# Kernel tuning notes

Measured on AMD Instinct MI355X. Metric: run time of the kernel, lower is better.

The kernel has to match this reference:

```python
import jax, jax.numpy as jnp
import numpy as np

EPS = 1e-12  # F.normalize eps


def _gather_nb(var, idx):
    # var: [B, N, C], idx: [B, N, K] -> [B, N, K, C]; out[b,n,k,c] = var[b, idx[b,n,k], c]
    return jnp.take_along_axis(var[:, :, None, :], idx[:, :, :, None], axis=1)


def _l2norm(v):
    n = jnp.sqrt(jnp.sum(v * v, axis=-1, keepdims=True))
    return v / jnp.maximum(n, EPS)


def setup_inputs() -> dict:
    key = jax.random.key(0)
    ks = jax.random.split(key, 16)
    B, N, K, dim, hid = 4, 4096, 16, 128, 64
    s = 0.05
    return {
        "pos": jax.random.normal(ks[0], (B, N, 3), jnp.float32),
        "x": jax.random.normal(ks[1], (B, dim, N), jnp.float32),
        "idx": jax.random.randint(ks[2], (B, N, K), 0, N, jnp.int64),
        "dist": jax.random.uniform(ks[3], (B, N, K), jnp.float32),
        "W_qkv": jax.random.normal(ks[4], (3 * dim, dim), jnp.float32) * s,
        "W1": jax.random.normal(ks[5], (hid, 10), jnp.float32) * s,
        "b1": jax.random.normal(ks[6], (hid,), jnp.float32) * s,
        "W2": jax.random.normal(ks[7], (dim, hid), jnp.float32) * s,
        "b2": jax.random.normal(ks[8], (dim,), jnp.float32) * s,
        "Wm1": jax.random.normal(ks[9], (4 * dim, dim), jnp.float32) * s,
        "bm1": jax.random.normal(ks[10], (4 * dim,), jnp.float32) * s,
        "Wm2": jax.random.normal(ks[11], (dim, 4 * dim), jnp.float32) * s,
        "bm2": jax.random.normal(ks[12], (dim,), jnp.float32) * s,
    }


def reference(pos, x, idx, dist, W_qkv, W1, b1, W2, b2, Wm1, bm1, Wm2, bm2):
    B, _, N = x.shape
    xt = jnp.transpose(x, (0, 2, 1))                      # [B, N, C]
    qkv = xt @ W_qkv.T                                    # [B, N, 3C]
    Q, K_, V = jnp.split(qkv, 3, axis=-1)

    Qg = _gather_nb(Q, idx)                               # [B, N, K, C]
    Kg = _gather_nb(K_, idx)
    Vg = _gather_nb(V, idx)

    # position embedding: [center(3) | neighbor(3) | diff(3) | dist(1)] -> MLP 10->hid->C
    pos_nb = _gather_nb(pos, idx)                         # [B, N, K, 3]
    pos_c = jnp.broadcast_to(pos[:, :, None, :], pos_nb.shape)
    feat10 = jnp.concatenate(
        [pos_c, pos_nb, pos_c - pos_nb, dist[..., None]], axis=-1)  # [B, N, K, 10]
    pos_emb = jax.nn.relu(feat10 @ W1.T + b1) @ W2.T + b2  # [B, N, K, C]

    Knorm = _l2norm(Kg + pos_emb)                         # [B, N, K, C]
    Vrel = jax.nn.relu(Vg + pos_emb)                      # [B, N, K, C]
    Qn = _l2norm(Qg)                                      # [B, N, K, C]

    # kv_context: contract over N per neighbor slot k -> [B, K, C, C]
    kv = jnp.einsum('bnkc,bnkd->bkcd', Knorm, Vrel)
    # (1/N) Qn @ kv, then sum over k -> [B, N, C]
    agg = jnp.einsum('bnkc,bkcd->bnd', Qn, kv) / N

    out = jax.nn.relu(agg @ Wm1.T + bm1) @ Wm2.T + bm2 + xt  # [B, N, C]
    return jnp.transpose(out, (0, 2, 1))                     # [B, C, N]
```

## Files before the change

kernel.cpp:

```cpp
#include <hip/hip_runtime.h>
#include <math.h>

#define Bn 4
#define Nn 4096
#define Kn 16
#define Cn 128
#define HIDn 64

#define OFF_WQKVBF 0
#define OFF_WM1BF  24576
#define OFF_WM2BF  57344
#define OFF_W2BFG  90112
#define OFF_QNBF   94208
#define OFF_KMBF   1142784
#define OFF_VMBF   2191360
#define OFF_KVT32  3239936
#define OFF_KVTBF  4288512
#define OFF_AGG0   4812800
#define OFF_AGG1   6909952
#define OFF_FLAG   9007104

typedef short bf16x8 __attribute__((ext_vector_type(8)));
typedef float f32x4 __attribute__((ext_vector_type(4)));

__device__ inline unsigned short f2bf(float f) {
  union { float f; unsigned u; } v; v.f = f;
  unsigned r = v.u + 0x7fffu + ((v.u >> 16) & 1u);
  return (unsigned short)(r >> 16);
}
__device__ inline float b2f(unsigned short s) {
  union { unsigned u; float f; } v; v.u = ((unsigned)s) << 16; return v.f;
}

__global__ void k0_prep(const float* __restrict__ Wqkv,
                        const float* __restrict__ Wm1, const float* __restrict__ Wm2,
                        const float* __restrict__ W2,
                        const int* __restrict__ idx_raw, float* ws) {
  if (blockIdx.x == 0 && threadIdx.x == 0) {
    int any = 0;
    for (int i = 0; i < 64; ++i) any |= idx_raw[2 * i + 1];
    ((int*)(ws + OFF_FLAG))[0] = (any == 0) ? 1 : 0;
  }
  int t = blockIdx.x * 256 + threadIdx.x;
  if (t < 49152) { ((unsigned short*)(ws + OFF_WQKVBF))[t] = f2bf(Wqkv[t]); return; }
  t -= 49152;
  if (t < 65536) { ((unsigned short*)(ws + OFF_WM1BF))[t] = f2bf(Wm1[t]); return; }
  t -= 65536;
  if (t < 65536) { ((unsigned short*)(ws + OFF_WM2BF))[t] = f2bf(Wm2[t]); return; }
  t -= 65536;
  if (t < 8192) { ((unsigned short*)(ws + OFF_W2BFG))[t] = f2bf(W2[t]); return; }
}

__global__ __launch_bounds__(256, 2) void k1_qkv(const float* __restrict__ x, float* ws) {
  __shared__ __align__(16) unsigned short a_lds[32 * 136];
  __shared__ __align__(16) float qkv_lds[32 * 388];
  const unsigned short* Wq = (const unsigned short*)(ws + OFF_WQKVBF);
  unsigned short* Qnbf = (unsigned short*)(ws + OFF_QNBF);
  unsigned short* KmBF = (unsigned short*)(ws + OFF_KMBF);
  unsigned short* VmBF = (unsigned short*)(ws + OFF_VMBF);
  int b = blockIdx.x >> 7;
  int n0 = (blockIdx.x & 127) << 5;
  int t = threadIdx.x;
  int w = t >> 6, l = t & 63, ml = l & 15, gq = l >> 4;
#pragma unroll
  for (int i = 0; i < 16; ++i) {
    int id = t + 256 * i;
    int c = id >> 5, j = id & 31;
    a_lds[j * 136 + c] = f2bf(x[(b * Cn + c) * Nn + n0 + j]);
  }
  __syncthreads();
  f32x4 acc[2][6];
#pragma unroll
  for (int i = 0; i < 2; ++i)
#pragma unroll
    for (int j = 0; j < 6; ++j) acc[i][j] = (f32x4)0.f;
#pragma unroll
  for (int kc = 0; kc < 4; ++kc) {
    bf16x8 av0 = *(const bf16x8*)&a_lds[ml * 136 + kc * 32 + 8 * gq];
    bf16x8 av1 = *(const bf16x8*)&a_lds[(ml + 16) * 136 + kc * 32 + 8 * gq];
#pragma unroll
    for (int nf = 0; nf < 6; ++nf) {
      int m = 96 * w + 16 * nf + ml;
      bf16x8 bv = *(const bf16x8*)&Wq[m * 128 + kc * 32 + 8 * gq];
      acc[0][nf] = __builtin_amdgcn_mfma_f32_16x16x32_bf16(av0, bv, acc[0][nf], 0, 0, 0);
      acc[1][nf] = __builtin_amdgcn_mfma_f32_16x16x32_bf16(av1, bv, acc[1][nf], 0, 0, 0);
    }
  }
#pragma unroll
  for (int mf = 0; mf < 2; ++mf)
#pragma unroll
    for (int nf = 0; nf < 6; ++nf)
#pragma unroll
      for (int r = 0; r < 4; ++r)
        qkv_lds[(16 * mf + 4 * gq + r) * 388 + 96 * w + 16 * nf + ml] = acc[mf][nf][r];
  __syncthreads();
  {
    int g = t >> 3, l8 = t & 7;
    float4 q4[4];
    float ss = 0.f;
#pragma unroll
    for (int q = 0; q < 4; ++q) {
      q4[q] = *(const float4*)&qkv_lds[g * 388 + l8 * 16 + 4 * q];
      ss = fmaf(q4[q].x, q4[q].x, ss); ss = fmaf(q4[q].y, q4[q].y, ss);
      ss = fmaf(q4[q].z, q4[q].z, ss); ss = fmaf(q4[q].w, q4[q].w, ss);
    }
    ss += __shfl_xor(ss, 1); ss += __shfl_xor(ss, 2); ss += __shfl_xor(ss, 4);
    float sc = 1.f / fmaxf(sqrtf(ss), 1e-12f);
    union { unsigned short us[8]; uint4 u4; } o0, o1;
#pragma unroll
    for (int q = 0; q < 2; ++q) {
      o0.us[q * 4 + 0] = f2bf(q4[q].x * sc); o0.us[q * 4 + 1] = f2bf(q4[q].y * sc);
      o0.us[q * 4 + 2] = f2bf(q4[q].z * sc); o0.us[q * 4 + 3] = f2bf(q4[q].w * sc);
    }
#pragma unroll
    for (int q = 0; q < 2; ++q) {
      o1.us[q * 4 + 0] = f2bf(q4[2 + q].x * sc); o1.us[q * 4 + 1] = f2bf(q4[2 + q].y * sc);
      o1.us[q * 4 + 2] = f2bf(q4[2 + q].z * sc); o1.us[q * 4 + 3] = f2bf(q4[2 + q].w * sc);
    }
    *(uint4*)&Qnbf[(b * Nn + n0 + g) * Cn + l8 * 16] = o0.u4;
    *(uint4*)&Qnbf[(b * Nn + n0 + g) * Cn + l8 * 16 + 8] = o1.u4;
  }
#pragma unroll
  for (int i = 0; i < 2; ++i) {
    int id = t + 256 * i;
    int row = id >> 4, c8 = id & 15;
    const float* kp = &qkv_lds[row * 388 + 128 + c8 * 8];
    const float* vp = &qkv_lds[row * 388 + 256 + c8 * 8];
    union { unsigned short us[8]; uint4 u4; } ko, vo;
#pragma unroll
    for (int j = 0; j < 8; ++j) { ko.us[j] = f2bf(kp[j]); vo.us[j] = f2bf(vp[j]); }
    *(uint4*)&KmBF[(b * Nn + n0 + row) * Cn + c8 * 8] = ko.u4;
    *(uint4*)&VmBF[(b * Nn + n0 + row) * Cn + c8 * 8] = vo.u4;
  }
}

#define CH2 8
__global__ __launch_bounds__(256, 2) void k2_kv(const float* __restrict__ pos,
                                                const float* __restrict__ dist,
                                                const int* __restrict__ idxp,
                                                const float* __restrict__ W1,
                                                const float* __restrict__ b1,
                                                const float* __restrict__ b2,
                                                float* ws) {
  __shared__ __align__(16) unsigned short h_lds[32 * 72];
  __shared__ __align__(16) unsigned short pe_bf[32 * 136];
  __shared__ __align__(16) unsigned short K_rm[32 * 136];
  __shared__ __align__(16) unsigned short V_rm[32 * 136];
  __shared__ __align__(16) unsigned short KnT[128 * 40];
  __shared__ __align__(16) unsigned short VrT[128 * 40];

  const unsigned short* KmBF = (const unsigned short*)(ws + OFF_KMBF);
  const unsigned short* VmBF = (const unsigned short*)(ws + OFF_VMBF);
  const unsigned short* W2g = (const unsigned short*)(ws + OFF_W2BFG);
  float* kvt = ws + OFF_KVT32;
  int flag = ((const int*)(ws + OFF_FLAG))[0];

  int bid = blockIdx.x;
  int b = bid & 3;
  int rest = bid >> 2;
  int k = rest & 15, ch = rest >> 4;
  int t = threadIdx.x;
  int w = t >> 6, l = t & 63;
  int ml = l & 15, gq = l >> 4;

  int g = t >> 3, l8 = t & 7;
  int nl = (t >> 3) & 7, half = t & 7;
  int n_b2 = 8 * w + nl;
  int side = t >> 7, cc = t & 127;

  f32x4 acc[2][8];
#pragma unroll
  for (int i = 0; i < 2; ++i)
#pragma unroll
    for (int j = 0; j < 8; ++j) acc[i][j] = (f32x4)0.f;

  int nbase = ch * 512;
  int fidx_m = (b * Nn + nbase + g) * Kn + k;
  int jn_m = flag ? idxp[2 * fidx_m] : idxp[fidx_m];
  float dd = dist[fidx_m];
  float pc0 = pos[(b * Nn + nbase + g) * 3 + 0];
  float pc1 = pos[(b * Nn + nbase + g) * 3 + 1];
  float pc2 = pos[(b * Nn + nbase + g) * 3 + 2];
  float pn0 = pos[(b * Nn + jn_m) * 3 + 0];
  float pn1 = pos[(b * Nn + jn_m) * 3 + 1];
  float pn2 = pos[(b * Nn + jn_m) * 3 + 2];
  int fidx_b = (b * Nn + nbase + n_b2) * Kn + k;
  int jn_b = flag ? idxp[2 * fidx_b] : idxp[fidx_b];
  union U8 { unsigned short us[8]; uint4 u4; };
  U8 ka, kb, va, vb;
  {
    const unsigned short* krow = &KmBF[(b * Nn + jn_b) * Cn];
    const unsigned short* vrow = &VmBF[(b * Nn + jn_b) * Cn];
    ka.u4 = *(const uint4*)&krow[half * 16];
    kb.u4 = *(const uint4*)&krow[half * 16 + 8];
    va.u4 = *(const uint4*)&vrow[half * 16];
    vb.u4 = *(const uint4*)&vrow[half * 16 + 8];
  }

  for (int it = 0; it < 16; ++it) {
    {
      float f10[10] = {pc0, pc1, pc2, pn0, pn1, pn2, pc0 - pn0, pc1 - pn1, pc2 - pn2, dd};
      union { unsigned short us[8]; uint4 u4; } hv;
#pragma unroll
      for (int oo = 0; oo < 8; ++oo) {
        int o = l8 * 8 + oo;
        float a = b1[o];
#pragma unroll
        for (int i2 = 0; i2 < 10; ++i2) a = fmaf(W1[o * 10 + i2], f10[i2], a);
        hv.us[oo] = f2bf(fmaxf(a, 0.f));
      }
      *(uint4*)&h_lds[g * 72 + l8 * 8] = hv.u4;
    }
    int itn = (it < 15) ? it + 1 : 15;
    int n0n = nbase + itn * 32;
    int fidx_mn = (b * Nn + n0n + g) * Kn + k;
    int jn_mn = flag ? idxp[2 * fidx_mn] : idxp[fidx_mn];
    float ddn = dist[fidx_mn];
    int fidx_bn = (b * Nn + n0n + n_b2) * Kn + k;
    int jn_bn = flag ? idxp[2 * fidx_bn] : idxp[fidx_bn];
    __syncthreads();
    {
      f32x4 pacc[2][2];
#pragma unroll
      for (int i = 0; i < 2; ++i)
#pragma unroll
        for (int j = 0; j < 2; ++j) pacc[i][j] = (f32x4)0.f;
#pragma unroll
      for (int hc = 0; hc < 64; hc += 32) {
        bf16x8 av[2];
#pragma unroll
        for (int mf = 0; mf < 2; ++mf)
          av[mf] = *(const bf16x8*)&h_lds[(ml + 16 * mf) * 72 + hc + 8 * gq];
#pragma unroll
        for (int nf = 0; nf < 2; ++nf) {
          int c = 32 * w + 16 * nf + ml;
          bf16x8 bv = *(const bf16x8*)&W2g[c * 64 + hc + 8 * gq];
          pacc[0][nf] = __builtin_amdgcn_mfma_f32_16x16x32_bf16(av[0], bv, pacc[0][nf], 0, 0, 0);
          pacc[1][nf] = __builtin_amdgcn_mfma_f32_16x16x32_bf16(av[1], bv, pacc[1][nf], 0, 0, 0);
        }
      }
#pragma unroll
      for (int mf = 0; mf < 2; ++mf)
#pragma unroll
        for (int nf = 0; nf < 2; ++nf) {
          int c = 32 * w + 16 * nf + ml;
#pragma unroll
          for (int r = 0; r < 4; ++r)
            pe_bf[(16 * mf + 4 * gq + r) * 136 + c] = f2bf(pacc[mf][nf][r]);
        }
    }
    __syncthreads();
    {
      U8 pa, pb;
      pa.u4 = *(const uint4*)&pe_bf[n_b2 * 136 + half * 16];
      pb.u4 = *(const uint4*)&pe_bf[n_b2 * 136 + half * 16 + 8];
      const float4* b2v4 = (const float4*)b2;
      float4 bz[4];
#pragma unroll
      for (int q = 0; q < 4; ++q) bz[q] = b2v4[half * 4 + q];
      float kr[16], vr[16];
      float ss = 0.f;
#pragma unroll
      for (int j = 0; j < 16; ++j) {
        float b2j = (j & 2) ? ((j & 1) ? bz[j >> 2].w : bz[j >> 2].z)
                            : ((j & 1) ? bz[j >> 2].y : bz[j >> 2].x);
        float pe = b2f((j < 8) ? pa.us[j] : pb.us[j - 8]) + b2j;
        float kg = b2f((j < 8) ? ka.us[j] : kb.us[j - 8]);
        float vg = b2f((j < 8) ? va.us[j] : vb.us[j - 8]);
        kr[j] = kg + pe;
        vr[j] = fmaxf(vg + pe, 0.f);
        ss = fmaf(kr[j], kr[j], ss);
      }
      ss += __shfl_xor(ss, 1); ss += __shfl_xor(ss, 2); ss += __shfl_xor(ss, 4);
      float sc = 1.f / fmaxf(sqrtf(ss), 1e-12f);
      union { unsigned short us[8]; uint4 u4; } o;
#pragma unroll
      for (int hh = 0; hh < 2; ++hh) {
#pragma unroll
        for (int j = 0; j < 8; ++j) o.us[j] = f2bf(kr[hh * 8 + j] * sc);
        *(uint4*)&K_rm[n_b2 * 136 + half * 16 + 8 * hh] = o.u4;
      }
#pragma unroll
      for (int hh = 0; hh < 2; ++hh) {
#pragma unroll
        for (int j = 0; j < 8; ++j) o.us[j] = f2bf(vr[hh * 8 + j]);
        *(uint4*)&V_rm[n_b2 * 136 + half * 16 + 8 * hh] = o.u4;
      }
    }
    float pc0n = pos[(b * Nn + n0n + g) * 3 + 0];
    float pc1n = pos[(b * Nn + n0n + g) * 3 + 1];
    float pc2n = pos[(b * Nn + n0n + g) * 3 + 2];
    float pn0n = pos[(b * Nn + jn_mn) * 3 + 0];
    float pn1n = pos[(b * Nn + jn_mn) * 3 + 1];
    float pn2n = pos[(b * Nn + jn_mn) * 3 + 2];
    U8 kan, kbn, van, vbn;
    {
      const unsigned short* krow = &KmBF[(b * Nn + jn_bn) * Cn];
      const unsigned short* vrow = &VmBF[(b * Nn + jn_bn) * Cn];
      kan.u4 = *(const uint4*)&krow[half * 16];
      kbn.u4 = *(const uint4*)&krow[half * 16 + 8];
      van.u4 = *(const uint4*)&vrow[half * 16];
      vbn.u4 = *(const uint4*)&vrow[half * 16 + 8];
    }
    __syncthreads();
    {
      const unsigned short* src = side ? V_rm : K_rm;
      unsigned short* dst = side ? VrT : KnT;
      unsigned v[16];
#pragma unroll
      for (int i = 0; i < 16; ++i) {
        unsigned lo = src[(2 * i) * 136 + cc];
        unsigned hi = src[(2 * i + 1) * 136 + cc];
        v[i] = lo | (hi << 16);
      }
#pragma unroll
      for (int i = 0; i < 4; ++i) {
        uint4 pk = {v[4 * i], v[4 * i + 1], v[4 * i + 2], v[4 * i + 3]};
        *(uint4*)&dst[cc * 40 + 8 * i] = pk;
      }
    }
    __syncthreads();
    {
      bf16x8 av[2];
#pragma unroll
      for (int mf = 0; mf < 2; ++mf)
        av[mf] = *(const bf16x8*)&VrT[(32 * w + 16 * mf + ml) * 40 + 8 * gq];
#pragma unroll
      for (int nf = 0; nf < 8; ++nf) {
        bf16x8 bv = *(const bf16x8*)&KnT[(16 * nf + ml) * 40 + 8 * gq];
#pragma unroll
        for (int mf = 0; mf < 2; ++mf)
          acc[mf][nf] = __builtin_amdgcn_mfma_f32_16x16x32_bf16(av[mf], bv, acc[mf][nf], 0, 0, 0);
      }
    }
    dd = ddn;
    pc0 = pc0n; pc1 = pc1n; pc2 = pc2n;
    pn0 = pn0n; pn1 = pn1n; pn2 = pn2n;
    ka.u4 = kan.u4; kb.u4 = kbn.u4; va.u4 = van.u4; vb.u4 = vbn.u4;
  }
  float* kvp = kvt + (b * Kn + k) * Cn * Cn;
#pragma unroll
  for (int mf = 0; mf < 2; ++mf)
#pragma unroll
    for (int nf = 0; nf < 8; ++nf) {
      int c = 16 * nf + ml;
#pragma unroll
      for (int r = 0; r < 4; ++r) {
        int d = 32 * w + 16 * mf + 4 * gq + r;
        atomicAdd(&kvp[d * Cn + c], acc[mf][nf][r]);
      }
    }
}

__global__ __launch_bounds__(256) void k2b_cvt(float* ws) {
  const float* src = ws + OFF_KVT32;
  unsigned short* dst = (unsigned short*)(ws + OFF_KVTBF);
  int i = blockIdx.x * 256 + threadIdx.x;
  float4 a = *(const float4*)&src[i * 8];
  float4 c = *(const float4*)&src[i * 8 + 4];
  union { unsigned short us[8]; uint4 u4; } o;
  o.us[0] = f2bf(a.x); o.us[1] = f2bf(a.y); o.us[2] = f2bf(a.z); o.us[3] = f2bf(a.w);
  o.us[4] = f2bf(c.x); o.us[5] = f2bf(c.y); o.us[6] = f2bf(c.z); o.us[7] = f2bf(c.w);
  *(uint4*)&dst[i * 8] = o.u4;
}

__global__ __launch_bounds__(256, 4) void k3_agg(const int* __restrict__ idxp, float* ws) {
  __shared__ __align__(16) unsigned short qt[32 * 136];
  const unsigned short* Qnbf = (const unsigned short*)(ws + OFF_QNBF);
  const unsigned short* kvtbf = (const unsigned short*)(ws + OFF_KVTBF);
  int flag = ((const int*)(ws + OFF_FLAG))[0];

  int bid = blockIdx.x;
  int b = bid & 3;
  int kh = (bid >> 2) & 1;
  int nt = bid >> 3;
  int n0 = nt * 32;
  int t = threadIdx.x;
  int w = t >> 6, l = t & 63;
  int ml = l & 15, gq = l >> 4;

  f32x4 acc[2][2];
#pragma unroll
  for (int i = 0; i < 2; ++i)
#pragma unroll
    for (int j = 0; j < 2; ++j) acc[i][j] = (f32x4)0.f;

  for (int kk = 0; kk < 8; ++kk) {
    int k = kh * 8 + kk;
    __syncthreads();
#pragma unroll
    for (int i = 0; i < 2; ++i) {
      int id = t + 256 * i;
      int row = id >> 4, c16 = id & 15;
      int fidx = (b * Nn + n0 + row) * Kn + k;
      int jn = flag ? idxp[2 * fidx] : idxp[fidx];
      uint4 v = *(const uint4*)&Qnbf[(b * Nn + jn) * Cn + c16 * 8];
      *(uint4*)&qt[row * 136 + c16 * 8] = v;
    }
    __syncthreads();
    const unsigned short* kvp = &kvtbf[(b * Kn + k) * Cn * Cn];
#pragma unroll
    for (int c0 = 0; c0 < 128; c0 += 32) {
      bf16x8 a0 = *(const bf16x8*)&qt[ml * 136 + c0 + 8 * gq];
      bf16x8 a1 = *(const bf16x8*)&qt[(ml + 16) * 136 + c0 + 8 * gq];
#pragma unroll
      for (int nf = 0; nf < 2; ++nf) {
        int d = 32 * w + 16 * nf + ml;
        bf16x8 bv = *(const bf16x8*)&kvp[d * Cn + c0 + 8 * gq];
        acc[0][nf] = __builtin_amdgcn_mfma_f32_16x16x32_bf16(a0, bv, acc[0][nf], 0, 0, 0);
        acc[1][nf] = __builtin_amdgcn_mfma_f32_16x16x32_bf16(a1, bv, acc[1][nf], 0, 0, 0);
      }
    }
  }
  float* ag = ws + (kh ? OFF_AGG1 : OFF_AGG0);
#pragma unroll
  for (int mf = 0; mf < 2; ++mf)
#pragma unroll
    for (int nf = 0; nf < 2; ++nf) {
      int d = 32 * w + 16 * nf + ml;
#pragma unroll
      for (int r = 0; r < 4; ++r) {
        int n = n0 + 16 * mf + 4 * gq + r;
        ag[(b * Nn + n) * Cn + d] = acc[mf][nf][r];
      }
    }
}

__global__ __launch_bounds__(256, 2) void k4_mlp(const float* __restrict__ x,
                                                 const float* __restrict__ bm1,
                                                 const float* __restrict__ bm2,
                                                 float* __restrict__ out, float* ws) {
  __shared__ __align__(16) unsigned short a_lds[32 * 136];
  __shared__ __align__(16) unsigned short h_lds[32 * 520];
  __shared__ float out_s[128 * 33];
  const float* agg0 = ws + OFF_AGG0;
  const float* agg1 = ws + OFF_AGG1;
  const unsigned short* Wm1bf = (const unsigned short*)(ws + OFF_WM1BF);
  const unsigned short* Wm2bf = (const unsigned short*)(ws + OFF_WM2BF);
  const float invN = 1.f / (float)Nn;
  int b = blockIdx.x >> 7;
  int n0 = (blockIdx.x & 127) << 5;
  int t = threadIdx.x;
  int w = t >> 6, l = t & 63, ml = l & 15, gq = l >> 4;
#pragma unroll
  for (int i = 0; i < 4; ++i) {
    int id = t + 256 * i;
    int row = id >> 5, c4 = id & 31;
    int off = (b * Nn + n0 + row) * Cn + c4 * 4;
    float4 v0 = *(const float4*)&agg0[off];
    float4 v1 = *(const float4*)&agg1[off];
    union { unsigned short us[4]; uint2 u2; } o;
    o.us[0] = f2bf((v0.x + v1.x) * invN); o.us[1] = f2bf((v0.y + v1.y) * invN);
    o.us[2] = f2bf((v0.z + v1.z) * invN); o.us[3] = f2bf((v0.w + v1.w) * invN);
    *(uint2*)&a_lds[row * 136 + c4 * 4] = o.u2;
  }
  __syncthreads();
  {
    f32x4 hacc[2][8];
#pragma unroll
    for (int i = 0; i < 2; ++i)
#pragma unroll
      for (int j = 0; j < 8; ++j) hacc[i][j] = (f32x4)0.f;
#pragma unroll
    for (int kc = 0; kc < 4; ++kc) {
      bf16x8 av0 = *(const bf16x8*)&a_lds[ml * 136 + kc * 32 + 8 * gq];
      bf16x8 av1 = *(const bf16x8*)&a_lds[(ml + 16) * 136 + kc * 32 + 8 * gq];
#pragma unroll
      for (int nf = 0; nf < 8; ++nf) {
        int h = 128 * w + 16 * nf + ml;
        bf16x8 bv = *(const bf16x8*)&Wm1bf[h * 128 + kc * 32 + 8 * gq];
        hacc[0][nf] = __builtin_amdgcn_mfma_f32_16x16x32_bf16(av0, bv, hacc[0][nf], 0, 0, 0);
        hacc[1][nf] = __builtin_amdgcn_mfma_f32_16x16x32_bf16(av1, bv, hacc[1][nf], 0, 0, 0);
      }
    }
#pragma unroll
    for (int mf = 0; mf < 2; ++mf)
#pragma unroll
      for (int nf = 0; nf < 8; ++nf) {
        int h = 128 * w + 16 * nf + ml;
        float bias = bm1[h];
#pragma unroll
        for (int r = 0; r < 4; ++r)
          h_lds[(16 * mf + 4 * gq + r) * 520 + h] = f2bf(fmaxf(hacc[mf][nf][r] + bias, 0.f));
      }
  }
  __syncthreads();
  {
    f32x4 oacc[2][2];
#pragma unroll
    for (int i = 0; i < 2; ++i)
#pragma unroll
      for (int j = 0; j < 2; ++j) oacc[i][j] = (f32x4)0.f;
#pragma unroll
    for (int kc = 0; kc < 16; ++kc) {
      bf16x8 av0 = *(const bf16x8*)&h_lds[ml * 520 + kc * 32 + 8 * gq];
      bf16x8 av1 = *(const bf16x8*)&h_lds[(ml + 16) * 520 + kc * 32 + 8 * gq];
#pragma unroll
      for (int nf = 0; nf < 2; ++nf) {
        int co = 32 * w + 16 * nf + ml;
        bf16x8 bv = *(const bf16x8*)&Wm2bf[co * 512 + kc * 32 + 8 * gq];
        oacc[0][nf] = __builtin_amdgcn_mfma_f32_16x16x32_bf16(av0, bv, oacc[0][nf], 0, 0, 0);
        oacc[1][nf] = __builtin_amdgcn_mfma_f32_16x16x32_bf16(av1, bv, oacc[1][nf], 0, 0, 0);
      }
    }
#pragma unroll
    for (int mf = 0; mf < 2; ++mf)
#pragma unroll
      for (int nf = 0; nf < 2; ++nf) {
        int co = 32 * w + 16 * nf + ml;
        float bias = bm2[co];
#pragma unroll
        for (int r = 0; r < 4; ++r)
          out_s[co * 33 + 16 * mf + 4 * gq + r] = oacc[mf][nf][r] + bias;
      }
  }
  __syncthreads();
#pragma unroll
  for (int i = 0; i < 16; ++i) {
    int id = t + 256 * i;
    int co = id >> 5, j = id & 31;
    out[(b * Cn + co) * Nn + n0 + j] = out_s[co * 33 + j] + x[(b * Cn + co) * Nn + n0 + j];
  }
}

extern "C" void kernel_launch(void* const* d_in, const int* in_sizes, int n_in,
                              void* d_out, int out_size, void* d_ws, size_t ws_size,
                              hipStream_t stream) {
  const float* pos  = (const float*)d_in[0];
  const float* x    = (const float*)d_in[1];
  const int*   idx  = (const int*)d_in[2];
  const float* dist = (const float*)d_in[3];
  const float* Wqkv = (const float*)d_in[4];
  const float* W1   = (const float*)d_in[5];
  const float* b1   = (const float*)d_in[6];
  const float* W2   = (const float*)d_in[7];
  const float* b2   = (const float*)d_in[8];
  const float* Wm1  = (const float*)d_in[9];
  const float* bm1  = (const float*)d_in[10];
  const float* Wm2  = (const float*)d_in[11];
  const float* bm2  = (const float*)d_in[12];
  float* out = (float*)d_out;
  float* ws = (float*)d_ws;

  hipMemsetAsync(ws + OFF_KVT32, 0, (size_t)Bn * Kn * Cn * Cn * sizeof(float), stream);
  hipLaunchKernelGGL(k0_prep, dim3(736), dim3(256), 0, stream, Wqkv, Wm1, Wm2, W2, idx, ws);
  hipLaunchKernelGGL(k1_qkv, dim3(Bn * 128), dim3(256), 0, stream, x, ws);
  hipLaunchKernelGGL(k2_kv, dim3(Bn * Kn * CH2), dim3(256), 0, stream, pos, dist, idx, W1, b1, b2, ws);
  hipLaunchKernelGGL(k2b_cvt, dim3(512), dim3(256), 0, stream, ws);
  hipLaunchKernelGGL(k3_agg, dim3(Bn * 2 * 128), dim3(256), 0, stream, idx, ws);
  hipLaunchKernelGGL(k4_mlp, dim3(Bn * 128), dim3(256), 0, stream, x, bm1, bm2, out, ws);
}
```

Baseline: 167.2 us.

## Compute position-MLP first layer with MFMA and fold biases into epilogues

The scalar FMA loop for the 10->64 position-embedding layer, which read W1 from global memory on every iteration, is replaced by bf16 MFMA over a zero-padded 32-wide feature tile kept in LDS. A new padded bf16 copy of W1 is built in the prep kernel. Biases b1 and b2 are loaded once into registers and added in the MFMA epilogues, and the position gathers are now done by only 32 threads per block. Launch bounds are raised to 3 blocks per CU. The first layer now runs in bf16 (features and weights rounded), which loses some precision, and an extra barrier is added per iteration.

```diff
diff --git a/kernel.cpp b/kernel.cpp
--- a/kernel.cpp
+++ b/kernel.cpp
@@ -11,14 +11,15 @@
 #define OFF_WM1BF  24576
 #define OFF_WM2BF  57344
 #define OFF_W2BFG  90112
-#define OFF_QNBF   94208
-#define OFF_KMBF   1142784
-#define OFF_VMBF   2191360
-#define OFF_KVT32  3239936
-#define OFF_KVTBF  4288512
-#define OFF_AGG0   4812800
-#define OFF_AGG1   6909952
-#define OFF_FLAG   9007104
+#define OFF_W1PBF  94208
+#define OFF_QNBF   95232
+#define OFF_KMBF   1143808
+#define OFF_VMBF   2192384
+#define OFF_KVT32  3240960
+#define OFF_KVTBF  4289536
+#define OFF_AGG0   4813824
+#define OFF_AGG1   6910976
+#define OFF_FLAG   9008128
 
 typedef short bf16x8 __attribute__((ext_vector_type(8)));
 typedef float f32x4 __attribute__((ext_vector_type(4)));
@@ -34,7 +35,7 @@
 
 __global__ void k0_prep(const float* __restrict__ Wqkv,
                         const float* __restrict__ Wm1, const float* __restrict__ Wm2,
-                        const float* __restrict__ W2,
+                        const float* __restrict__ W2, const float* __restrict__ W1,
                         const int* __restrict__ idx_raw, float* ws) {
   if (blockIdx.x == 0 && threadIdx.x == 0) {
     int any = 0;
@@ -49,6 +50,12 @@
   if (t < 65536) { ((unsigned short*)(ws + OFF_WM2BF))[t] = f2bf(Wm2[t]); return; }
   t -= 65536;
   if (t < 8192) { ((unsigned short*)(ws + OFF_W2BFG))[t] = f2bf(W2[t]); return; }
+  t -= 8192;
+  if (t < 2048) {
+    int o = t >> 5, i = t & 31;
+    ((unsigned short*)(ws + OFF_W1PBF))[t] = (i < 10) ? f2bf(W1[o * 10 + i]) : 0;
+    return;
+  }
 }
 
 __global__ __launch_bounds__(256, 2) void k1_qkv(const float* __restrict__ x, float* ws) {
@@ -135,13 +142,13 @@
 }
 
 #define CH2 8
-__global__ __launch_bounds__(256, 2) void k2_kv(const float* __restrict__ pos,
+__global__ __launch_bounds__(256, 3) void k2_kv(const float* __restrict__ pos,
                                                 const float* __restrict__ dist,
                                                 const int* __restrict__ idxp,
-                                                const float* __restrict__ W1,
                                                 const float* __restrict__ b1,
                                                 const float* __restrict__ b2,
                                                 float* ws) {
+  __shared__ __align__(16) unsigned short feat[32 * 40];
   __shared__ __align__(16) unsigned short h_lds[32 * 72];
   __shared__ __align__(16) unsigned short pe_bf[32 * 136];
   __shared__ __align__(16) unsigned short K_rm[32 * 136];
@@ -152,6 +159,7 @@
   const unsigned short* KmBF = (const unsigned short*)(ws + OFF_KMBF);
   const unsigned short* VmBF = (const unsigned short*)(ws + OFF_VMBF);
   const unsigned short* W2g = (const unsigned short*)(ws + OFF_W2BFG);
+  const unsigned short* W1P = (const unsigned short*)(ws + OFF_W1PBF);
   float* kvt = ws + OFF_KVT32;
   int flag = ((const int*)(ws + OFF_FLAG))[0];
 
@@ -163,10 +171,14 @@
   int w = t >> 6, l = t & 63;
   int ml = l & 15, gq = l >> 4;
 
-  int g = t >> 3, l8 = t & 7;
   int nl = (t >> 3) & 7, half = t & 7;
   int n_b2 = 8 * w + nl;
   int side = t >> 7, cc = t & 127;
+  bool is32 = (t < 32);
+
+  float b1v = b1[16 * w + ml];
+  float b2v0 = b2[32 * w + ml];
+  float b2v1 = b2[32 * w + 16 + ml];
 
   f32x4 acc[2][8];
 #pragma unroll
@@ -175,18 +187,22 @@
     for (int j = 0; j < 8; ++j) acc[i][j] = (f32x4)0.f;
 
   int nbase = ch * 512;
-  int fidx_m = (b * Nn + nbase + g) * Kn + k;
-  int jn_m = flag ? idxp[2 * fidx_m] : idxp[fidx_m];
-  float dd = dist[fidx_m];
-  float pc0 = pos[(b * Nn + nbase + g) * 3 + 0];
-  float pc1 = pos[(b * Nn + nbase + g) * 3 + 1];
-  float pc2 = pos[(b * Nn + nbase + g) * 3 + 2];
-  float pn0 = pos[(b * Nn + jn_m) * 3 + 0];
-  float pn1 = pos[(b * Nn + jn_m) * 3 + 1];
-  float pn2 = pos[(b * Nn + jn_m) * 3 + 2];
+  union U8 { unsigned short us[8]; uint4 u4; };
+
+  float dd = 0.f, pc0 = 0.f, pc1 = 0.f, pc2 = 0.f, pn0 = 0.f, pn1 = 0.f, pn2 = 0.f;
+  if (is32) {
+    int fidx_m = (b * Nn + nbase + t) * Kn + k;
+    int jn_m = flag ? idxp[2 * fidx_m] : idxp[fidx_m];
+    dd = dist[fidx_m];
+    pc0 = pos[(b * Nn + nbase + t) * 3 + 0];
+    pc1 = pos[(b * Nn + nbase + t) * 3 + 1];
+    pc2 = pos[(b * Nn + nbase + t) * 3 + 2];
+    pn0 = pos[(b * Nn + jn_m) * 3 + 0];
+    pn1 = pos[(b * Nn + jn_m) * 3 + 1];
+    pn2 = pos[(b * Nn + jn_m) * 3 + 2];
+  }
   int fidx_b = (b * Nn + nbase + n_b2) * Kn + k;
   int jn_b = flag ? idxp[2 * fidx_b] : idxp[fidx_b];
-  union U8 { unsigned short us[8]; uint4 u4; };
   U8 ka, kb, va, vb;
   {
     const unsigned short* krow = &KmBF[(b * Nn + jn_b) * Cn];
@@ -196,26 +212,46 @@
     va.u4 = *(const uint4*)&vrow[half * 16];
     vb.u4 = *(const uint4*)&vrow[half * 16 + 8];
   }
+  if (is32) {
+    float f10[10] = {pc0, pc1, pc2, pn0, pn1, pn2, pc0 - pn0, pc1 - pn1, pc2 - pn2, dd};
+    U8 f0, f1, z;
+#pragma unroll
+    for (int j = 0; j < 8; ++j) f0.us[j] = f2bf(f10[j]);
+    f1.us[0] = f2bf(f10[8]); f1.us[1] = f2bf(f10[9]);
+#pragma unroll
+    for (int j = 2; j < 8; ++j) f1.us[j] = 0;
+#pragma unroll
+    for (int j = 0; j < 8; ++j) z.us[j] = 0;
+    *(uint4*)&feat[t * 40] = f0.u4;
+    *(uint4*)&feat[t * 40 + 8] = f1.u4;
+    *(uint4*)&feat[t * 40 + 16] = z.u4;
+    *(uint4*)&feat[t * 40 + 24] = z.u4;
+  }
 
   for (int it = 0; it < 16; ++it) {
+    __syncthreads();
     {
-      float f10[10] = {pc0, pc1, pc2, pn0, pn1, pn2, pc0 - pn0, pc1 - pn1, pc2 - pn2, dd};
-      union { unsigned short us[8]; uint4 u4; } hv;
-#pragma unroll
-      for (int oo = 0; oo < 8; ++oo) {
-        int o = l8 * 8 + oo;
-        float a = b1[o];
-#pragma unroll
-        for (int i2 = 0; i2 < 10; ++i2) a = fmaf(W1[o * 10 + i2], f10[i2], a);
-        hv.us[oo] = f2bf(fmaxf(a, 0.f));
-      }
-      *(uint4*)&h_lds[g * 72 + l8 * 8] = hv.u4;
+      bf16x8 fa0 = *(const bf16x8*)&feat[ml * 40 + 8 * gq];
+      bf16x8 fa1 = *(const bf16x8*)&feat[(ml + 16) * 40 + 8 * gq];
+      bf16x8 wv = *(const bf16x8*)&W1P[(16 * w + ml) * 32 + 8 * gq];
+      f32x4 h0 = (f32x4)0.f, h1 = (f32x4)0.f;
+      h0 = __builtin_amdgcn_mfma_f32_16x16x32_bf16(fa0, wv, h0, 0, 0, 0);
+      h1 = __builtin_amdgcn_mfma_f32_16x16x32_bf16(fa1, wv, h1, 0, 0, 0);
+#pragma unroll
+      for (int r = 0; r < 4; ++r) {
+        h_lds[(4 * gq + r) * 72 + 16 * w + ml] = f2bf(fmaxf(h0[r] + b1v, 0.f));
+        h_lds[(16 + 4 * gq + r) * 72 + 16 * w + ml] = f2bf(fmaxf(h1[r] + b1v, 0.f));
+      }
     }
     int itn = (it < 15) ? it + 1 : 15;
     int n0n = nbase + itn * 32;
-    int fidx_mn = (b * Nn + n0n + g) * Kn + k;
-    int jn_mn = flag ? idxp[2 * fidx_mn] : idxp[fidx_mn];
-    float ddn = dist[fidx_mn];
+    int jn_mn = 0;
+    float ddn = 0.f;
+    if (is32) {
+      int fidx_mn = (b * Nn + n0n + t) * Kn + k;
+      jn_mn = flag ? idxp[2 * fidx_mn] : idxp[fidx_mn];
+      ddn = dist[fidx_mn];
+    }
     int fidx_bn = (b * Nn + n0n + n_b2) * Kn + k;
     int jn_bn = flag ? idxp[2 * fidx_bn] : idxp[fidx_bn];
     __syncthreads();
@@ -244,9 +280,10 @@
 #pragma unroll
         for (int nf = 0; nf < 2; ++nf) {
           int c = 32 * w + 16 * nf + ml;
+          float bias = nf ? b2v1 : b2v0;
 #pragma unroll
           for (int r = 0; r < 4; ++r)
-            pe_bf[(16 * mf + 4 * gq + r) * 136 + c] = f2bf(pacc[mf][nf][r]);
+            pe_bf[(16 * mf + 4 * gq + r) * 136 + c] = f2bf(pacc[mf][nf][r] + bias);
         }
     }
     __syncthreads();
@@ -254,17 +291,11 @@
       U8 pa, pb;
       pa.u4 = *(const uint4*)&pe_bf[n_b2 * 136 + half * 16];
       pb.u4 = *(const uint4*)&pe_bf[n_b2 * 136 + half * 16 + 8];
-      const float4* b2v4 = (const float4*)b2;
-      float4 bz[4];
-#pragma unroll
-      for (int q = 0; q < 4; ++q) bz[q] = b2v4[half * 4 + q];
       float kr[16], vr[16];
       float ss = 0.f;
 #pragma unroll
       for (int j = 0; j < 16; ++j) {
-        float b2j = (j & 2) ? ((j & 1) ? bz[j >> 2].w : bz[j >> 2].z)
-                            : ((j & 1) ? bz[j >> 2].y : bz[j >> 2].x);
-        float pe = b2f((j < 8) ? pa.us[j] : pb.us[j - 8]) + b2j;
+        float pe = b2f((j < 8) ? pa.us[j] : pb.us[j - 8]);
         float kg = b2f((j < 8) ? ka.us[j] : kb.us[j - 8]);
         float vg = b2f((j < 8) ? va.us[j] : vb.us[j - 8]);
         kr[j] = kg + pe;
@@ -287,12 +318,15 @@
         *(uint4*)&V_rm[n_b2 * 136 + half * 16 + 8 * hh] = o.u4;
       }
     }
-    float pc0n = pos[(b * Nn + n0n + g) * 3 + 0];
-    float pc1n = pos[(b * Nn + n0n + g) * 3 + 1];
-    float pc2n = pos[(b * Nn + n0n + g) * 3 + 2];
-    float pn0n = pos[(b * Nn + jn_mn) * 3 + 0];
-    float pn1n = pos[(b * Nn + jn_mn) * 3 + 1];
-    float pn2n = pos[(b * Nn + jn_mn) * 3 + 2];
+    float pc0n = 0.f, pc1n = 0.f, pc2n = 0.f, pn0n = 0.f, pn1n = 0.f, pn2n = 0.f;
+    if (is32) {
+      pc0n = pos[(b * Nn + n0n + t) * 3 + 0];
+      pc1n = pos[(b * Nn + n0n + t) * 3 + 1];
+      pc2n = pos[(b * Nn + n0n + t) * 3 + 2];
+      pn0n = pos[(b * Nn + jn_mn) * 3 + 0];
+      pn1n = pos[(b * Nn + jn_mn) * 3 + 1];
+      pn2n = pos[(b * Nn + jn_mn) * 3 + 2];
+    }
     U8 kan, kbn, van, vbn;
     {
       const unsigned short* krow = &KmBF[(b * Nn + jn_bn) * Cn];
@@ -333,9 +367,22 @@
           acc[mf][nf] = __builtin_amdgcn_mfma_f32_16x16x32_bf16(av[mf], bv, acc[mf][nf], 0, 0, 0);
       }
     }
-    dd = ddn;
-    pc0 = pc0n; pc1 = pc1n; pc2 = pc2n;
-    pn0 = pn0n; pn1 = pn1n; pn2 = pn2n;
+    if (is32) {
+      float f10[10] = {pc0n, pc1n, pc2n, pn0n, pn1n, pn2n,
+                       pc0n - pn0n, pc1n - pn1n, pc2n - pn2n, ddn};
+      U8 f0, f1, z;
+#pragma unroll
+      for (int j = 0; j < 8; ++j) f0.us[j] = f2bf(f10[j]);
+      f1.us[0] = f2bf(f10[8]); f1.us[1] = f2bf(f10[9]);
+#pragma unroll
+      for (int j = 2; j < 8; ++j) f1.us[j] = 0;
+#pragma unroll
+      for (int j = 0; j < 8; ++j) z.us[j] = 0;
+      *(uint4*)&feat[t * 40] = f0.u4;
+      *(uint4*)&feat[t * 40 + 8] = f1.u4;
+      *(uint4*)&feat[t * 40 + 16] = z.u4;
+      *(uint4*)&feat[t * 40 + 24] = z.u4;
+    }
     ka.u4 = kan.u4; kb.u4 = kbn.u4; va.u4 = van.u4; vb.u4 = vbn.u4;
   }
   float* kvp = kvt + (b * Kn + k) * Cn * Cn;
@@ -543,9 +590,9 @@
   float* ws = (float*)d_ws;
 
   hipMemsetAsync(ws + OFF_KVT32, 0, (size_t)Bn * Kn * Cn * Cn * sizeof(float), stream);
-  hipLaunchKernelGGL(k0_prep, dim3(736), dim3(256), 0, stream, Wqkv, Wm1, Wm2, W2, idx, ws);
+  hipLaunchKernelGGL(k0_prep, dim3(744), dim3(256), 0, stream, Wqkv, Wm1, Wm2, W2, W1, idx, ws);
   hipLaunchKernelGGL(k1_qkv, dim3(Bn * 128), dim3(256), 0, stream, x, ws);
-  hipLaunchKernelGGL(k2_kv, dim3(Bn * Kn * CH2), dim3(256), 0, stream, pos, dist, idx, W1, b1, b2, ws);
+  hipLaunchKernelGGL(k2_kv, dim3(Bn * Kn * CH2), dim3(256), 0, stream, pos, dist, idx, b1, b2, ws);
   hipLaunchKernelGGL(k2b_cvt, dim3(512), dim3(256), 0, stream, ws);
   hipLaunchKernelGGL(k3_agg, dim3(Bn * 2 * 128), dim3(256), 0, stream, idx, ws);
   hipLaunchKernelGGL(k4_mlp, dim3(Bn * 128), dim3(256), 0, stream, x, bm1, bm2, out, ws);
```

Result: slower. 172.3 us (+3.0%).

## Double-buffer transposed K/V tiles and defer kv MFMA to next iteration

Applied to the files above, without the earlier changes.

Double-buffers the transposed KnT/VrT shared tiles in k2_kv. The kv MFMA for tile it-1 now runs at the start of iteration it, which removes one __syncthreads per iteration and lets that MFMA overlap the position-embedding work; a final MFMA after the loop handles the last tile. It also folds the b2 bias into the bf16 conversion of the position embedding instead of reloading b2 per element. Shared memory grows by about 20KB per block, which may limit occupancy at two blocks per CU. Adding the bias before bf16 rounding changes rounding slightly. The workspace offsets shift by 1024 floats.

```diff
diff --git a/kernel.cpp b/kernel.cpp
--- a/kernel.cpp
+++ b/kernel.cpp
@@ -11,14 +11,14 @@
 #define OFF_WM1BF  24576
 #define OFF_WM2BF  57344
 #define OFF_W2BFG  90112
-#define OFF_QNBF   94208
-#define OFF_KMBF   1142784
-#define OFF_VMBF   2191360
-#define OFF_KVT32  3239936
-#define OFF_KVTBF  4288512
-#define OFF_AGG0   4812800
-#define OFF_AGG1   6909952
-#define OFF_FLAG   9007104
+#define OFF_QNBF   95232
+#define OFF_KMBF   1143808
+#define OFF_VMBF   2192384
+#define OFF_KVT32  3240960
+#define OFF_KVTBF  4289536
+#define OFF_AGG0   4813824
+#define OFF_AGG1   6910976
+#define OFF_FLAG   9008128
 
 typedef short bf16x8 __attribute__((ext_vector_type(8)));
 typedef float f32x4 __attribute__((ext_vector_type(4)));
@@ -146,8 +146,8 @@
   __shared__ __align__(16) unsigned short pe_bf[32 * 136];
   __shared__ __align__(16) unsigned short K_rm[32 * 136];
   __shared__ __align__(16) unsigned short V_rm[32 * 136];
-  __shared__ __align__(16) unsigned short KnT[128 * 40];
-  __shared__ __align__(16) unsigned short VrT[128 * 40];
+  __shared__ __align__(16) unsigned short KnT[2][128 * 40];
+  __shared__ __align__(16) unsigned short VrT[2][128 * 40];
 
   const unsigned short* KmBF = (const unsigned short*)(ws + OFF_KMBF);
   const unsigned short* VmBF = (const unsigned short*)(ws + OFF_VMBF);
@@ -168,6 +168,9 @@
   int n_b2 = 8 * w + nl;
   int side = t >> 7, cc = t & 127;
 
+  float b2v0 = b2[32 * w + ml];
+  float b2v1 = b2[32 * w + 16 + ml];
+
   f32x4 acc[2][8];
 #pragma unroll
   for (int i = 0; i < 2; ++i)
@@ -175,6 +178,8 @@
     for (int j = 0; j < 8; ++j) acc[i][j] = (f32x4)0.f;
 
   int nbase = ch * 512;
+  union U8 { unsigned short us[8]; uint4 u4; };
+
   int fidx_m = (b * Nn + nbase + g) * Kn + k;
   int jn_m = flag ? idxp[2 * fidx_m] : idxp[fidx_m];
   float dd = dist[fidx_m];
@@ -186,7 +191,6 @@
   float pn2 = pos[(b * Nn + jn_m) * 3 + 2];
   int fidx_b = (b * Nn + nbase + n_b2) * Kn + k;
   int jn_b = flag ? idxp[2 * fidx_b] : idxp[fidx_b];
-  union U8 { unsigned short us[8]; uint4 u4; };
   U8 ka, kb, va, vb;
   {
     const unsigned short* krow = &KmBF[(b * Nn + jn_b) * Cn];
@@ -219,6 +223,21 @@
     int fidx_bn = (b * Nn + n0n + n_b2) * Kn + k;
     int jn_bn = flag ? idxp[2 * fidx_bn] : idxp[fidx_bn];
     __syncthreads();
+    if (it > 0) {
+      const unsigned short* ktp = KnT[(it - 1) & 1];
+      const unsigned short* vtp = VrT[(it - 1) & 1];
+      bf16x8 av[2];
+#pragma unroll
+      for (int mf = 0; mf < 2; ++mf)
+        av[mf] = *(const bf16x8*)&vtp[(32 * w + 16 * mf + ml) * 40 + 8 * gq];
+#pragma unroll
+      for (int nf = 0; nf < 8; ++nf) {
+        bf16x8 bv = *(const bf16x8*)&ktp[(16 * nf + ml) * 40 + 8 * gq];
+#pragma unroll
+        for (int mf = 0; mf < 2; ++mf)
+          acc[mf][nf] = __builtin_amdgcn_mfma_f32_16x16x32_bf16(av[mf], bv, acc[mf][nf], 0, 0, 0);
+      }
+    }
     {
       f32x4 pacc[2][2];
 #pragma unroll
@@ -244,9 +263,10 @@
 #pragma unroll
         for (int nf = 0; nf < 2; ++nf) {
           int c = 32 * w + 16 * nf + ml;
+          float bias = nf ? b2v1 : b2v0;
 #pragma unroll
           for (int r = 0; r < 4; ++r)
-            pe_bf[(16 * mf + 4 * gq + r) * 136 + c] = f2bf(pacc[mf][nf][r]);
+            pe_bf[(16 * mf + 4 * gq + r) * 136 + c] = f2bf(pacc[mf][nf][r] + bias);
         }
     }
     __syncthreads();
@@ -254,17 +274,11 @@
       U8 pa, pb;
       pa.u4 = *(const uint4*)&pe_bf[n_b2 * 136 + half * 16];
       pb.u4 = *(const uint4*)&pe_bf[n_b2 * 136 + half * 16 + 8];
-      const float4* b2v4 = (const float4*)b2;
-      float4 bz[4];
-#pragma unroll
-      for (int q = 0; q < 4; ++q) bz[q] = b2v4[half * 4 + q];
       float kr[16], vr[16];
       float ss = 0.f;
 #pragma unroll
       for (int j = 0; j < 16; ++j) {
-        float b2j = (j & 2) ? ((j & 1) ? bz[j >> 2].w : bz[j >> 2].z)
-                            : ((j & 1) ? bz[j >> 2].y : bz[j >> 2].x);
-        float pe = b2f((j < 8) ? pa.us[j] : pb.us[j - 8]) + b2j;
+        float pe = b2f((j < 8) ? pa.us[j] : pb.us[j - 8]);
         float kg = b2f((j < 8) ? ka.us[j] : kb.us[j - 8]);
         float vg = b2f((j < 8) ? va.us[j] : vb.us[j - 8]);
         kr[j] = kg + pe;
@@ -305,7 +319,7 @@
     __syncthreads();
     {
       const unsigned short* src = side ? V_rm : K_rm;
-      unsigned short* dst = side ? VrT : KnT;
+      unsigned short* dst = side ? VrT[it & 1] : KnT[it & 1];
       unsigned v[16];
 #pragma unroll
       for (int i = 0; i < 16; ++i) {
@@ -319,24 +333,26 @@
         *(uint4*)&dst[cc * 40 + 8 * i] = pk;
       }
     }
-    __syncthreads();
-    {
-      bf16x8 av[2];
-#pragma unroll
-      for (int mf = 0; mf < 2; ++mf)
-        av[mf] = *(const bf16x8*)&VrT[(32 * w + 16 * mf + ml) * 40 + 8 * gq];
-#pragma unroll
-      for (int nf = 0; nf < 8; ++nf) {
-        bf16x8 bv = *(const bf16x8*)&KnT[(16 * nf + ml) * 40 + 8 * gq];
-#pragma unroll
-        for (int mf = 0; mf < 2; ++mf)
-          acc[mf][nf] = __builtin_amdgcn_mfma_f32_16x16x32_bf16(av[mf], bv, acc[mf][nf], 0, 0, 0);
-      }
-    }
     dd = ddn;
     pc0 = pc0n; pc1 = pc1n; pc2 = pc2n;
     pn0 = pn0n; pn1 = pn1n; pn2 = pn2n;
     ka.u4 = kan.u4; kb.u4 = kbn.u4; va.u4 = van.u4; vb.u4 = vbn.u4;
+  }
+  __syncthreads();
+  {
+    const unsigned short* ktp = KnT[15 & 1];
+    const unsigned short* vtp = VrT[15 & 1];
+    bf16x8 av[2];
+#pragma unroll
+    for (int mf = 0; mf < 2; ++mf)
+      av[mf] = *(const bf16x8*)&vtp[(32 * w + 16 * mf + ml) * 40 + 8 * gq];
+#pragma unroll
+    for (int nf = 0; nf < 8; ++nf) {
+      bf16x8 bv = *(const bf16x8*)&ktp[(16 * nf + ml) * 40 + 8 * gq];
+#pragma unroll
+      for (int mf = 0; mf < 2; ++mf)
+        acc[mf][nf] = __builtin_amdgcn_mfma_f32_16x16x32_bf16(av[mf], bv, acc[mf][nf], 0, 0, 0);
+    }
   }
   float* kvp = kvt + (b * Kn + k) * Cn * Cn;
 #pragma unroll
```

Result: faster. 160.3 us (-4.1%).
